# Performance work log

Measured on AMD Instinct MI355X. Metric: run time of the kernel, lower is better.

The kernel has to match this reference:

```python
import jax, jax.numpy as jnp
import numpy as np

H = 128        # hidden_dim
R = 50         # num_rbf
L = 4          # num_layers
CUTOFF = 5.0
N = 10000      # atoms
M = 64         # molecules
BOX = 54.7     # box side -> ~32 neighbors within cutoff
EPS = 1e-5     # LayerNorm eps (torch default)


def setup_inputs() -> dict:
    rng = np.random.default_rng(0)
    positions = rng.uniform(0.0, BOX, size=(N, 3)).astype(np.float32)
    # static radius graph (the torch module filters a dense NxN pair list by cutoff;
    # we do that once here so runtime shapes are fixed / jit-friendly)
    sq = (positions ** 2).sum(-1)
    d2 = sq[:, None] + sq[None, :] - 2.0 * positions @ positions.T
    mask = (d2 < CUTOFF * CUTOFF) & ~np.eye(N, dtype=bool)
    row, col = np.nonzero(mask)
    edge_index = jnp.asarray(np.stack([row, col]).astype(np.int32))  # [2, E]

    key = jax.random.key(0)
    ks = jax.random.split(key, 6)
    s = 0.05
    return dict(
        atomic_numbers=jax.random.randint(ks[0], (N,), 0, 100),
        positions=jnp.asarray(positions),
        batch=jnp.asarray((np.arange(N) * M // N).astype(np.int32)),  # sorted, all M present
        edge_index=edge_index,
        embedding=jax.random.normal(ks[1], (100, H), jnp.float32) * s,
        W1=jax.random.normal(ks[2], (L, H + R, H), jnp.float32) * s,
        b1=jnp.zeros((L, H), jnp.float32),
        W2=jax.random.normal(ks[3], (L, H, H), jnp.float32) * s,
        b2=jnp.zeros((L, H), jnp.float32),
        W_ih=jax.random.normal(ks[4], (L, H, 3 * H), jnp.float32) * s,
        b_ih=jax.random.normal(ks[5], (L, 3 * H), jnp.float32) * s,
        b_hh=jnp.zeros((L, 3 * H), jnp.float32),
        ln_g=jnp.ones((H,), jnp.float32),
        ln_b=jnp.zeros((H,), jnp.float32),
    )


def reference(atomic_numbers, positions, batch, edge_index, embedding,
              W1, b1, W2, b2, W_ih, b_ih, b_hh, ln_g, ln_b):
    x = embedding[jnp.clip(atomic_numbers, 0, 99)]                  # [N, H]
    row, col = edge_index[0], edge_index[1]
    d = jnp.linalg.norm(positions[row] - positions[col], axis=-1)   # [E]
    centers = jnp.linspace(0.0, CUTOFF, R)
    width = CUTOFF / R
    rbf = jnp.exp(-((d[:, None] - centers) ** 2) / (2.0 * width * width))  # [E, R]
    n_atoms = x.shape[0]
    for l in range(L):
        x_j = x[row]                                                # gather [E, H]
        inp = jnp.concatenate([x_j, rbf], axis=-1)                  # [E, H+R]
        msg = jax.nn.silu(inp @ W1[l] + b1[l]) @ W2[l] + b2[l]      # [E, H]
        aggr = jax.ops.segment_sum(msg, col, num_segments=n_atoms)  # [N, H]
        # GRU step with h0 = 0: W_hh @ h vanishes, only b_hh survives
        gi = aggr @ W_ih[l] + b_ih[l]                               # [N, 3H]
        gi_r, gi_z, gi_n = jnp.split(gi, 3, axis=-1)
        bh_r, bh_z, bh_n = jnp.split(b_hh[l], 3)
        r = jax.nn.sigmoid(gi_r + bh_r)
        z = jax.nn.sigmoid(gi_z + bh_z)
        n = jnp.tanh(gi_n + r * bh_n)
        x = x + (1.0 - z) * n                                       # h' = (1-z)*n + z*0
    mu = x.mean(-1, keepdims=True)
    var = ((x - mu) ** 2).mean(-1, keepdims=True)
    x = (x - mu) / jnp.sqrt(var + EPS) * ln_g + ln_b
    sums = jax.ops.segment_sum(x, batch, num_segments=M)            # [M, H]
    counts = jax.ops.segment_sum(jnp.ones((x.shape[0],), jnp.float32), batch, num_segments=M)
    graph_rep = sums / jnp.clip(counts, 1.0)[:, None]
    return x, graph_rep
```

## Files before the change

### kernel.cpp

```cpp
#include <hip/hip_runtime.h>
#include <hip/hip_bf16.h>
#include <math.h>


#define HH 128
#define RR 50
#define LL 4
#define L2E 1.4426950408889634f

typedef __attribute__((ext_vector_type(8))) short short8;
typedef __attribute__((ext_vector_type(4))) float floatx4;

__device__ __forceinline__ unsigned short f2bf(float f) {
    unsigned u = __float_as_uint(f);
    unsigned r = (u + 0x7fffu + ((u >> 16) & 1u)) >> 16;
    return (unsigned short)r;
}
__device__ __forceinline__ unsigned pack_bf2(float lo, float hi) {
    unsigned u0 = __float_as_uint(lo) + 0x8000u;
    unsigned u1 = __float_as_uint(hi) + 0x8000u;
    return __builtin_amdgcn_perm(u1, u0, 0x07060302);
}
__device__ __forceinline__ float fast_sigmoid(float x) {
    return __builtin_amdgcn_rcpf(1.f + __builtin_amdgcn_exp2f(x * (-L2E)));
}
__device__ __forceinline__ float fast_tanh(float x) {
    x = fminf(fmaxf(x, -15.f), 15.f);
    float t = __builtin_amdgcn_exp2f(x * (2.f * L2E));
    return (t - 1.f) * __builtin_amdgcn_rcpf(t + 1.f);
}
__device__ __forceinline__ int imin(int a, int b) { return a < b ? a : b; }

__global__ __launch_bounds__(256) void prep_kernel(
    const int* __restrict__ an, const float* __restrict__ emb,
    float* __restrict__ X,
    const float* __restrict__ pos, const int* __restrict__ erow,
    const int* __restrict__ ecol, float* __restrict__ dist,
    int* __restrict__ rowptr, int* __restrict__ bptr,
    const int* __restrict__ batch,
    const float* __restrict__ W1, unsigned short* __restrict__ W1rT,
    unsigned short* __restrict__ W1xT,
    const float* __restrict__ W2, const float* __restrict__ Wih,
    unsigned short* __restrict__ WcT,
    const float* __restrict__ b2, float* __restrict__ P,
    int N, int E, int M)
{
    int gidx = blockIdx.x * 256 + threadIdx.x;
    int c0 = N * HH;
    if (gidx < c0) {
        int i = gidx >> 7, n = gidx & 127;
        int z = an[i];
        z = z < 0 ? 0 : (z > 99 ? 99 : z);
        X[gidx] = emb[z * HH + n];
        return;
    }
    gidx -= c0;
    int PT = E > N ? E : N;
    if (gidx < PT) {
        int i = gidx;
        if (i < E) {
            int rc = erow[i];
            int rp = (i > 0) ? erow[i - 1] : -1;
            for (int r = rp + 1; r <= rc; ++r) rowptr[r] = i;
            if (i == E - 1)
                for (int r = rc + 1; r <= N; ++r) rowptr[r] = E;
        }
        if (i < N) {
            int bc = batch[i];
            int bp = (i > 0) ? batch[i - 1] : -1;
            for (int m = bp + 1; m <= bc; ++m) bptr[m] = i;
            if (i == N - 1)
                for (int m = bc + 1; m <= M; ++m) bptr[m] = N;
        }
        return;
    }
    gidx -= PT;
    if (gidx < E) {
        int e = gidx;
        int r = erow[e], c = ecol[e];
        float dx = pos[r * 3 + 0] - pos[c * 3 + 0];
        float dy = pos[r * 3 + 1] - pos[c * 3 + 1];
        float dz = pos[r * 3 + 2] - pos[c * 3 + 2];
        dist[e] = sqrtf(dx * dx + dy * dy + dz * dz);
        return;
    }
    gidx -= E;
    if (gidx < LL * HH * 64) {
        int l = gidx >> 13, rem = gidx & 8191;
        int f = rem >> 9, lane2 = (rem >> 3) & 63, j = rem & 7;
        int nt = f >> 1, h = f & 1;
        int n = nt * 16 + (lane2 & 15);
        int k = h * 32 + (lane2 >> 4) * 8 + j;
        float v = (k < RR) ? W1[((size_t)l * 178 + 128 + k) * HH + n] : 0.f;
        W1rT[gidx] = f2bf(v);
        return;
    }
    gidx -= LL * HH * 64;
    if (gidx < LL * HH * HH) {
        int l = gidx >> 14, rem = gidx & 16383, n = rem >> 7, k = rem & 127;
        W1xT[gidx] = f2bf(W1[((size_t)l * 178 + k) * HH + n]);
        return;
    }
    gidx -= LL * HH * HH;
    if (gidx < LL * HH * 384) {
        int l = gidx / (HH * 384), rem = gidx % (HH * 384);
        int i = rem / 384, j = rem % 384;
        const float* w2row = W2 + ((size_t)l * HH + i) * HH;
        const float* wih = Wih + (size_t)l * HH * 384;
        float acc = 0.f;
#pragma unroll 4
        for (int k = 0; k < HH; ++k)
            acc = fmaf(w2row[k], wih[(size_t)k * 384 + j], acc);
        WcT[((size_t)l * 384 + j) * HH + i] = f2bf(acc);
        return;
    }
    gidx -= LL * HH * 384;
    if (gidx < LL * 384) {
        int l = gidx / 384, j = gidx % 384;
        const float* b2l = b2 + (size_t)l * HH;
        const float* wih = Wih + (size_t)l * HH * 384;
        float acc = 0.f;
#pragma unroll 4
        for (int k = 0; k < HH; ++k)
            acc = fmaf(b2l[k], wih[(size_t)k * 384 + j], acc);
        P[gidx] = acc;
    }
}

#define XAB 32
__global__ __launch_bounds__(256) void xw_kernel(
    const float* __restrict__ X, const float* __restrict__ W,
    const float* __restrict__ bias, unsigned short* __restrict__ XWb, int N)
{
    __shared__ __align__(16) float A[XAB][HH];
    int tid = threadIdx.x;
    int abase = blockIdx.x * XAB;
    for (int idx = tid; idx < XAB * HH; idx += 256) {
        int a = idx >> 7, k = idx & 127;
        A[a][k] = (abase + a < N) ? X[(size_t)(abase + a) * HH + k] : 0.f;
    }
    __syncthreads();
    int n = tid & 127, s = tid >> 7;
    float acc[16];
#pragma unroll
    for (int i = 0; i < 16; ++i) acc[i] = 0.f;
    for (int kc = 0; kc < 32; ++kc) {
        float w0 = W[(4 * kc + 0) * HH + n];
        float w1 = W[(4 * kc + 1) * HH + n];
        float w2 = W[(4 * kc + 2) * HH + n];
        float w3 = W[(4 * kc + 3) * HH + n];
#pragma unroll
        for (int i = 0; i < 16; ++i) {
            float4 av = *(const float4*)&A[s * 16 + i][4 * kc];
            acc[i] = fmaf(av.x, w0, acc[i]);
            acc[i] = fmaf(av.y, w1, acc[i]);
            acc[i] = fmaf(av.z, w2, acc[i]);
            acc[i] = fmaf(av.w, w3, acc[i]);
        }
    }
    float b = bias[n];
#pragma unroll
    for (int i = 0; i < 16; ++i) {
        int a = abase + s * 16 + i;
        if (a < N) XWb[(size_t)a * HH + n] = f2bf(acc[i] + b);
    }
}

__global__ __launch_bounds__(256) void edge_mfma_kernel(
    const unsigned short* __restrict__ XWb, const unsigned short* __restrict__ W1rTf,
    const float* __restrict__ dist, const int* __restrict__ rowptr,
    const int* __restrict__ ecol, unsigned short* __restrict__ Sbf,
    int N, int nwaves)
{
    __shared__ __align__(16) unsigned short W1s[8192];
    int tid = threadIdx.x;
    {
        const uint4* src = (const uint4*)W1rTf;
        uint4* dst = (uint4*)W1s;
#pragma unroll
        for (int i = 0; i < 4; ++i) dst[tid + i * 256] = src[tid + i * 256];
    }
    __syncthreads();

    int wid = (blockIdx.x << 2) + (tid >> 6);
    int lane = tid & 63;
    int c = lane & 15, q = lane >> 4;

    const float stepc = 5.0f / 49.0f;
    const float negc = -50.f * L2E;
    float kqs = (float)(q << 3) * stepc;

    int NW = 2 * N;
    for (int w = wid; w < NW; w += nwaves) {
        int a = w >> 1, h = w & 1;
        int es = rowptr[a], ee = rowptr[a + 1];
        float acc[4][4];
#pragma unroll
        for (int t = 0; t < 4; ++t)
#pragma unroll
            for (int r = 0; r < 4; ++r) acc[t][r] = 0.f;

        if (es < ee) {
            int last = ee - 1;
            int ce0 = imin(es + c, last);
            float dcur = dist[ce0];
            int colcur = ecol[ce0];
            int ce1 = imin(es + 16 + c, last);
            float dnxt = dist[ce1];
            int colnxt = ecol[ce1];

            for (int eb = es; eb < ee; eb += 16) {
                const unsigned short* xwrow = XWb + (size_t)colcur * HH + h * 64;
                uint2 gx[4];
#pragma unroll
                for (int t = 0; t < 4; ++t)
                    gx[t] = *(const uint2*)&xwrow[t * 16 + (q << 2)];

                float d_t = dcur;
                dcur = dnxt; colcur = colnxt;
                int ce2 = imin(eb + 32 + c, last);
                dnxt = dist[ce2];
                colnxt = ecol[ce2];

                float dq0 = d_t - kqs;
                float dq1 = dq0 - 32.f * stepc;
                union { unsigned u[4]; short8 s; } ub0, ub1;
#pragma unroll
                for (int p = 0; p < 4; ++p) {
                    float t0 = dq0 - (float)(2 * p) * stepc;
                    float t1 = dq0 - (float)(2 * p + 1) * stepc;
                    float e0f = __builtin_amdgcn_exp2f(negc * t0 * t0);
                    float e1f = __builtin_amdgcn_exp2f(negc * t1 * t1);
                    ub0.u[p] = pack_bf2(e0f, e1f);
                    float t2 = dq1 - (float)(2 * p) * stepc;
                    float t3 = dq1 - (float)(2 * p + 1) * stepc;
                    float e2f = __builtin_amdgcn_exp2f(negc * t2 * t2);
                    float e3f = __builtin_amdgcn_exp2f(negc * t3 * t3);
                    ub1.u[p] = pack_bf2(e2f, e3f);
                }
                short8 B0 = ub0.s, B1 = ub1.s;
                float msk = ((eb + c) < ee) ? 1.f : 0.f;

                unsigned wbyte = (unsigned)(lane * 16);
                asm volatile("" : "+v"(wbyte));
                const char* Wlp = (const char*)W1s + wbyte;

#pragma unroll
                for (int t = 0; t < 4; ++t) {
                    int f0 = (h * 4 + t) * 2;
                    short8 A0 = *(const short8*)(Wlp + f0 * 1024);
                    short8 A1 = *(const short8*)(Wlp + (f0 + 1) * 1024);
                    floatx4 C;
                    C[0] = __uint_as_float(gx[t].x << 16);
                    C[1] = __uint_as_float(gx[t].x & 0xffff0000u);
                    C[2] = __uint_as_float(gx[t].y << 16);
                    C[3] = __uint_as_float(gx[t].y & 0xffff0000u);
                    C = __builtin_amdgcn_mfma_f32_16x16x32_bf16(A0, B0, C, 0, 0, 0);
                    C = __builtin_amdgcn_mfma_f32_16x16x32_bf16(A1, B1, C, 0, 0, 0);
#pragma unroll
                    for (int r = 0; r < 4; ++r) {
                        float hh = C[r];
                        float v = hh * fast_sigmoid(hh);
                        acc[t][r] = fmaf(v, msk, acc[t][r]);
                    }
                }
            }
        }

        int b0 = c & 1, b1 = (c >> 1) & 1, b2 = (c >> 2) & 1, b3 = (c >> 3) & 1;
        float s1[4][2];
#pragma unroll
        for (int t = 0; t < 4; ++t)
#pragma unroll
            for (int p = 0; p < 2; ++p) {
                float keep = b0 ? acc[t][2 * p + 1] : acc[t][2 * p];
                float send = b0 ? acc[t][2 * p] : acc[t][2 * p + 1];
                s1[t][p] = keep + __shfl_xor(send, 1, 64);
            }
        float s2[4];
#pragma unroll
        for (int t = 0; t < 4; ++t) {
            float keep = b1 ? s1[t][1] : s1[t][0];
            float send = b1 ? s1[t][0] : s1[t][1];
            s2[t] = keep + __shfl_xor(send, 2, 64);
        }
        float s3[2];
#pragma unroll
        for (int u = 0; u < 2; ++u) {
            float keep = b2 ? s2[2 * u + 1] : s2[2 * u];
            float send = b2 ? s2[2 * u] : s2[2 * u + 1];
            s3[u] = keep + __shfl_xor(send, 4, 64);
        }
        float keep = b3 ? s3[1] : s3[0];
        float send = b3 ? s3[0] : s3[1];
        float fin = keep + __shfl_xor(send, 8, 64);

        int t_fin = 2 * b3 + b2;
        int r_fin = 2 * b1 + b0;
        int n = t_fin * 16 + (q << 2) + r_fin;
        Sbf[(size_t)a * HH + h * 64 + n] = f2bf(fin);
    }
}

#define GA 16
__global__ __launch_bounds__(512) void grux_mfma_kernel(
    const unsigned short* __restrict__ Sbf, const unsigned short* __restrict__ WcT,
    const float* __restrict__ P, const float* __restrict__ bih,
    const float* __restrict__ bhh, const int* __restrict__ rowptr,
    float* __restrict__ X, int N,
    const unsigned short* __restrict__ W1xT, const float* __restrict__ b1next,
    unsigned short* __restrict__ XWb, int do_xw)
{
    __shared__ __align__(16) unsigned short Sb[GA][136];
    __shared__ __align__(16) unsigned short Xb[GA][136];
    int tid = threadIdx.x;
    int abase = blockIdx.x * GA;
    int w = tid >> 6, lane = tid & 63, c = lane & 15, q = lane >> 4;
    int n = w * 16 + c;

    float pn0 = P[n],        pn1 = P[128 + n],   pn2 = P[256 + n];
    float bi0 = bih[n],      bi1 = bih[128 + n], bi2 = bih[256 + n];
    float bh0 = bhh[n],      bh1 = bhh[128 + n], bh2 = bhh[256 + n];
    float deg[4];
#pragma unroll
    for (int r = 0; r < 4; ++r) {
        int a = abase + q * 4 + r;
        deg[r] = (a < N) ? (float)(rowptr[a + 1] - rowptr[a]) : 0.f;
    }

    if (tid < 128) {
        int a = tid >> 3, ch = tid & 7;
        int aa = abase + a; if (aa >= N) aa = N - 1;
        const uint4* src = (const uint4*)(Sbf + (size_t)aa * HH + ch * 16);
        uint4 v0 = src[0];
        uint4 v1 = src[1];
        uint4* dst = (uint4*)&Sb[a][ch * 16];
        dst[0] = v0;
        dst[1] = v1;
    }
    __syncthreads();

    floatx4 Cg0 = {0.f,0.f,0.f,0.f}, Cg1 = {0.f,0.f,0.f,0.f}, Cg2 = {0.f,0.f,0.f,0.f};
#pragma unroll
    for (int kt = 0; kt < 4; ++kt) {
        short8 A = *(const short8*)&Sb[c][kt * 32 + q * 8];
        short8 B0 = *(const short8*)&WcT[(size_t)(0 * 128 + n) * HH + kt * 32 + q * 8];
        short8 B1 = *(const short8*)&WcT[(size_t)(1 * 128 + n) * HH + kt * 32 + q * 8];
        short8 B2 = *(const short8*)&WcT[(size_t)(2 * 128 + n) * HH + kt * 32 + q * 8];
        Cg0 = __builtin_amdgcn_mfma_f32_16x16x32_bf16(A, B0, Cg0, 0, 0, 0);
        Cg1 = __builtin_amdgcn_mfma_f32_16x16x32_bf16(A, B1, Cg1, 0, 0, 0);
        Cg2 = __builtin_amdgcn_mfma_f32_16x16x32_bf16(A, B2, Cg2, 0, 0, 0);
    }

#pragma unroll
    for (int r = 0; r < 4; ++r) {
        int am = q * 4 + r;
        int a = abase + am;
        bool ok = a < N;
        float g0 = Cg0[r] + deg[r] * pn0 + bi0;
        float g1 = Cg1[r] + deg[r] * pn1 + bi1;
        float g2 = Cg2[r] + deg[r] * pn2 + bi2;
        float rr = fast_sigmoid(g0 + bh0);
        float zz = fast_sigmoid(g1 + bh1);
        float nn = fast_tanh(g2 + rr * bh2);
        float xv = 0.f;
        if (ok) {
            xv = X[(size_t)a * HH + n] + (1.f - zz) * nn;
            X[(size_t)a * HH + n] = xv;
        }
        Xb[am][n] = f2bf(xv);
    }

    if (!do_xw) return;
    __syncthreads();

    floatx4 Cx = {0.f, 0.f, 0.f, 0.f};
#pragma unroll
    for (int kt = 0; kt < 4; ++kt) {
        short8 A = *(const short8*)&Xb[c][kt * 32 + q * 8];
        short8 B = *(const short8*)&W1xT[(size_t)n * HH + kt * 32 + q * 8];
        Cx = __builtin_amdgcn_mfma_f32_16x16x32_bf16(A, B, Cx, 0, 0, 0);
    }
    float bn = b1next[n];
#pragma unroll
    for (int r = 0; r < 4; ++r) {
        int a = abase + q * 4 + r;
        if (a < N) XWb[(size_t)a * HH + n] = f2bf(Cx[r] + bn);
    }
}

__global__ __launch_bounds__(1024) void lnpool_kernel(
    const float* __restrict__ X, const float* __restrict__ g,
    const float* __restrict__ b, const int* __restrict__ bptr,
    float* __restrict__ outx, float* __restrict__ outg, int N)
{
    __shared__ float sm[16][128];
    int m = blockIdx.x, tid = threadIdx.x;
    int wv = tid >> 6, lane = tid & 63;
    int a0 = bptr[m], a1 = bptr[m + 1];
    float g0 = g[lane], g1 = g[64 + lane];
    float bb0 = b[lane], bb1 = b[64 + lane];
    float acc0 = 0.f, acc1 = 0.f;
    for (int a = a0 + wv; a < a1; a += 16) {
        float v0 = X[(size_t)a * HH + lane];
        float v1 = X[(size_t)a * HH + 64 + lane];
        float smv = v0 + v1;
        for (int off = 32; off > 0; off >>= 1) smv += __shfl_xor(smv, off, 64);
        float mu = smv * (1.f / 128.f);
        float d0 = v0 - mu, d1 = v1 - mu;
        float vq = d0 * d0 + d1 * d1;
        for (int off = 32; off > 0; off >>= 1) vq += __shfl_xor(vq, off, 64);
        float inv = rsqrtf(vq * (1.f / 128.f) + 1e-5f);
        float y0 = d0 * inv * g0 + bb0;
        float y1 = d1 * inv * g1 + bb1;
        outx[(size_t)a * HH + lane] = y0;
        outx[(size_t)a * HH + 64 + lane] = y1;
        acc0 += y0;
        acc1 += y1;
    }
    sm[wv][lane] = acc0;
    sm[wv][64 + lane] = acc1;
    __syncthreads();
    if (tid < 128) {
        float s = 0.f;
#pragma unroll
        for (int i = 0; i < 16; ++i) s += sm[i][tid];
        float cnt = (float)(a1 - a0);
        outg[(size_t)m * HH + tid] = s / fmaxf(cnt, 1.f);
    }
}

extern "C" void kernel_launch(void* const* d_in, const int* in_sizes, int n_in,
                              void* d_out, int out_size, void* d_ws, size_t ws_size,
                              hipStream_t stream)
{
    const int*   an   = (const int*)d_in[0];
    const float* pos  = (const float*)d_in[1];
    const int*   bat  = (const int*)d_in[2];
    const int*   eidx = (const int*)d_in[3];
    const float* emb  = (const float*)d_in[4];
    const float* W1   = (const float*)d_in[5];
    const float* b1   = (const float*)d_in[6];
    const float* W2   = (const float*)d_in[7];
    const float* b2   = (const float*)d_in[8];
    const float* Wih  = (const float*)d_in[9];
    const float* bih  = (const float*)d_in[10];
    const float* bhh  = (const float*)d_in[11];
    const float* lng  = (const float*)d_in[12];
    const float* lnb  = (const float*)d_in[13];

    int N = in_sizes[0];
    int E = in_sizes[3] / 2;
    int M = out_size / HH - N;
    const int* erow = eidx;
    const int* ecol = eidx + E;

    float* ws   = (float*)d_ws;
    size_t off = 0;
    float* X    = ws + off; off += (size_t)N * HH;
    unsigned short* Sbf = (unsigned short*)(ws + off); off += (size_t)N * HH / 2;
    unsigned short* XWb = (unsigned short*)(ws + off); off += (size_t)N * HH / 2;
    float* P    = ws + off; off += LL * 384;
    float* dist = ws + off; off += E;
    int* rowptr = (int*)(ws + off); off += N + 1;
    int* bptr   = (int*)(ws + off); off += M + 1;
    off = (off + 3) & ~(size_t)3;
    unsigned short* W1rT = (unsigned short*)(ws + off); off += (size_t)LL * HH * 32;
    unsigned short* W1xT = (unsigned short*)(ws + off); off += (size_t)LL * HH * 64;
    unsigned short* WcT  = (unsigned short*)(ws + off); off += (size_t)LL * 384 * 64;

    float* outx = (float*)d_out;
    float* outg = outx + (size_t)N * HH;

    int PT = (E > N ? E : N);
    long total = (long)N * HH + PT + E + LL * HH * 64 + LL * HH * HH
               + LL * HH * 384 + LL * 384;
    int prep_blocks = (int)((total + 255) / 256);

    prep_kernel<<<prep_blocks, 256, 0, stream>>>(
        an, emb, X, pos, erow, ecol, dist, rowptr, bptr, bat,
        W1, W1rT, W1xT, W2, Wih, WcT, b2, P, N, E, M);

    xw_kernel<<<(N + XAB - 1) / XAB, 256, 0, stream>>>(X, W1, b1, XWb, N);

    int eblocks = (2 * N + 3) / 4;
    int nwaves = eblocks * 4;
    int grux_blocks = (N + GA - 1) / GA;
    for (int l = 0; l < LL; ++l) {
        edge_mfma_kernel<<<eblocks, 256, 0, stream>>>(
            XWb, W1rT + (size_t)l * HH * 64, dist, rowptr, ecol, Sbf, N, nwaves);
        int do_xw = (l < LL - 1) ? 1 : 0;
        int ln = (l + 1 < LL) ? l + 1 : l;
        grux_mfma_kernel<<<grux_blocks, 512, 0, stream>>>(
            Sbf, WcT + (size_t)l * 384 * HH, P + l * 384,
            bih + l * 384, bhh + l * 384, rowptr, X, N,
            W1xT + (size_t)ln * HH * HH, b1 + (size_t)ln * HH, XWb, do_xw);
    }

    lnpool_kernel<<<M, 1024, 0, stream>>>(X, lng, lnb, bptr, outx, outg, N);
}
```

Baseline: 319.5 us.

## Fuse edge message kernel with GRU update into one per-layer kernel

Merges the edge aggregation kernel and the GRU/next-layer projection kernel into a single kernel per layer. Each 512-thread block handles 4 atoms, keeping the aggregated messages in shared memory instead of writing them to global memory, and ping-pongs the XW buffers across layers. This removes one launch per layer and the global round-trip of the aggregate. In exchange, the MFMA GRU stage now does 16-row tiles where only 4 rows are valid, and the W1 tile is reloaded into shared memory by four times as many blocks.

```diff
diff --git a/kernel.cpp b/kernel.cpp
--- a/kernel.cpp
+++ b/kernel.cpp
@@ -166,179 +166,163 @@
     }
 }
 
-__global__ __launch_bounds__(256) void edge_mfma_kernel(
-    const unsigned short* __restrict__ XWb, const unsigned short* __restrict__ W1rTf,
+__global__ __launch_bounds__(512) void fused_layer_kernel(
+    const unsigned short* __restrict__ XWin, const unsigned short* __restrict__ W1rTf,
     const float* __restrict__ dist, const int* __restrict__ rowptr,
-    const int* __restrict__ ecol, unsigned short* __restrict__ Sbf,
-    int N, int nwaves)
+    const int* __restrict__ ecol,
+    const unsigned short* __restrict__ WcT, const float* __restrict__ P,
+    const float* __restrict__ bih, const float* __restrict__ bhh,
+    float* __restrict__ X,
+    const unsigned short* __restrict__ W1xT, const float* __restrict__ b1next,
+    unsigned short* __restrict__ XWout, int do_xw, int N)
 {
     __shared__ __align__(16) unsigned short W1s[8192];
+    __shared__ __align__(16) unsigned short Sb[16][136];
+    __shared__ __align__(16) unsigned short Xb[16][136];
     int tid = threadIdx.x;
+    int abase = blockIdx.x * 4;
+    int w = tid >> 6, lane = tid & 63;
+    int c = lane & 15, q = lane >> 4;
+
     {
         const uint4* src = (const uint4*)W1rTf;
         uint4* dst = (uint4*)W1s;
-#pragma unroll
-        for (int i = 0; i < 4; ++i) dst[tid + i * 256] = src[tid + i * 256];
+        dst[tid] = src[tid];
+        dst[tid + 512] = src[tid + 512];
+        if (tid < 204) {
+            uint4 z; z.x = 0; z.y = 0; z.z = 0; z.w = 0;
+            ((uint4*)&Sb[4][0])[tid] = z;
+        }
     }
     __syncthreads();
 
-    int wid = (blockIdx.x << 2) + (tid >> 6);
-    int lane = tid & 63;
-    int c = lane & 15, q = lane >> 4;
-
-    const float stepc = 5.0f / 49.0f;
-    const float negc = -50.f * L2E;
-    float kqs = (float)(q << 3) * stepc;
-
-    int NW = 2 * N;
-    for (int w = wid; w < NW; w += nwaves) {
-        int a = w >> 1, h = w & 1;
-        int es = rowptr[a], ee = rowptr[a + 1];
+    {
+        int al = w >> 1, h = w & 1;
+        int a = abase + al;
         float acc[4][4];
 #pragma unroll
         for (int t = 0; t < 4; ++t)
 #pragma unroll
             for (int r = 0; r < 4; ++r) acc[t][r] = 0.f;
 
-        if (es < ee) {
-            int last = ee - 1;
-            int ce0 = imin(es + c, last);
-            float dcur = dist[ce0];
-            int colcur = ecol[ce0];
-            int ce1 = imin(es + 16 + c, last);
-            float dnxt = dist[ce1];
-            int colnxt = ecol[ce1];
-
-            for (int eb = es; eb < ee; eb += 16) {
-                const unsigned short* xwrow = XWb + (size_t)colcur * HH + h * 64;
-                uint2 gx[4];
-#pragma unroll
-                for (int t = 0; t < 4; ++t)
-                    gx[t] = *(const uint2*)&xwrow[t * 16 + (q << 2)];
-
-                float d_t = dcur;
-                dcur = dnxt; colcur = colnxt;
-                int ce2 = imin(eb + 32 + c, last);
-                dnxt = dist[ce2];
-                colnxt = ecol[ce2];
-
-                float dq0 = d_t - kqs;
-                float dq1 = dq0 - 32.f * stepc;
-                union { unsigned u[4]; short8 s; } ub0, ub1;
-#pragma unroll
-                for (int p = 0; p < 4; ++p) {
-                    float t0 = dq0 - (float)(2 * p) * stepc;
-                    float t1 = dq0 - (float)(2 * p + 1) * stepc;
-                    float e0f = __builtin_amdgcn_exp2f(negc * t0 * t0);
-                    float e1f = __builtin_amdgcn_exp2f(negc * t1 * t1);
-                    ub0.u[p] = pack_bf2(e0f, e1f);
-                    float t2 = dq1 - (float)(2 * p) * stepc;
-                    float t3 = dq1 - (float)(2 * p + 1) * stepc;
-                    float e2f = __builtin_amdgcn_exp2f(negc * t2 * t2);
-                    float e3f = __builtin_amdgcn_exp2f(negc * t3 * t3);
-                    ub1.u[p] = pack_bf2(e2f, e3f);
-                }
-                short8 B0 = ub0.s, B1 = ub1.s;
-                float msk = ((eb + c) < ee) ? 1.f : 0.f;
-
-                unsigned wbyte = (unsigned)(lane * 16);
-                asm volatile("" : "+v"(wbyte));
-                const char* Wlp = (const char*)W1s + wbyte;
-
-#pragma unroll
-                for (int t = 0; t < 4; ++t) {
-                    int f0 = (h * 4 + t) * 2;
-                    short8 A0 = *(const short8*)(Wlp + f0 * 1024);
-                    short8 A1 = *(const short8*)(Wlp + (f0 + 1) * 1024);
-                    floatx4 C;
-                    C[0] = __uint_as_float(gx[t].x << 16);
-                    C[1] = __uint_as_float(gx[t].x & 0xffff0000u);
-                    C[2] = __uint_as_float(gx[t].y << 16);
-                    C[3] = __uint_as_float(gx[t].y & 0xffff0000u);
-                    C = __builtin_amdgcn_mfma_f32_16x16x32_bf16(A0, B0, C, 0, 0, 0);
-                    C = __builtin_amdgcn_mfma_f32_16x16x32_bf16(A1, B1, C, 0, 0, 0);
-#pragma unroll
-                    for (int r = 0; r < 4; ++r) {
-                        float hh = C[r];
-                        float v = hh * fast_sigmoid(hh);
-                        acc[t][r] = fmaf(v, msk, acc[t][r]);
+        if (a < N) {
+            int es = rowptr[a], ee = rowptr[a + 1];
+            const float stepc = 5.0f / 49.0f;
+            const float negc = -50.f * L2E;
+            float kqs = (float)(q << 3) * stepc;
+            if (es < ee) {
+                int last = ee - 1;
+                int ce0 = imin(es + c, last);
+                float dcur = dist[ce0];
+                int colcur = ecol[ce0];
+                int ce1 = imin(es + 16 + c, last);
+                float dnxt = dist[ce1];
+                int colnxt = ecol[ce1];
+
+                for (int eb = es; eb < ee; eb += 16) {
+                    const unsigned short* xwrow = XWin + (size_t)colcur * HH + h * 64;
+                    uint2 gx[4];
+#pragma unroll
+                    for (int t = 0; t < 4; ++t)
+                        gx[t] = *(const uint2*)&xwrow[t * 16 + (q << 2)];
+
+                    float d_t = dcur;
+                    dcur = dnxt; colcur = colnxt;
+                    int ce2 = imin(eb + 32 + c, last);
+                    dnxt = dist[ce2];
+                    colnxt = ecol[ce2];
+
+                    float dq0 = d_t - kqs;
+                    float dq1 = dq0 - 32.f * stepc;
+                    union { unsigned u[4]; short8 s; } ub0, ub1;
+#pragma unroll
+                    for (int p = 0; p < 4; ++p) {
+                        float t0 = dq0 - (float)(2 * p) * stepc;
+                        float t1 = dq0 - (float)(2 * p + 1) * stepc;
+                        float e0f = __builtin_amdgcn_exp2f(negc * t0 * t0);
+                        float e1f = __builtin_amdgcn_exp2f(negc * t1 * t1);
+                        ub0.u[p] = pack_bf2(e0f, e1f);
+                        float t2 = dq1 - (float)(2 * p) * stepc;
+                        float t3 = dq1 - (float)(2 * p + 1) * stepc;
+                        float e2f = __builtin_amdgcn_exp2f(negc * t2 * t2);
+                        float e3f = __builtin_amdgcn_exp2f(negc * t3 * t3);
+                        ub1.u[p] = pack_bf2(e2f, e3f);
+                    }
+                    short8 B0 = ub0.s, B1 = ub1.s;
+                    float msk = ((eb + c) < ee) ? 1.f : 0.f;
+
+                    unsigned wbyte = (unsigned)(lane * 16);
+                    asm volatile("" : "+v"(wbyte));
+                    const char* Wlp = (const char*)W1s + wbyte;
+
+#pragma unroll
+                    for (int t = 0; t < 4; ++t) {
+                        int f0 = (h * 4 + t) * 2;
+                        short8 A0 = *(const short8*)(Wlp + f0 * 1024);
+                        short8 A1 = *(const short8*)(Wlp + (f0 + 1) * 1024);
+                        floatx4 C;
+                        C[0] = __uint_as_float(gx[t].x << 16);
+                        C[1] = __uint_as_float(gx[t].x & 0xffff0000u);
+                        C[2] = __uint_as_float(gx[t].y << 16);
+                        C[3] = __uint_as_float(gx[t].y & 0xffff0000u);
+                        C = __builtin_amdgcn_mfma_f32_16x16x32_bf16(A0, B0, C, 0, 0, 0);
+                        C = __builtin_amdgcn_mfma_f32_16x16x32_bf16(A1, B1, C, 0, 0, 0);
+#pragma unroll
+                        for (int r = 0; r < 4; ++r) {
+                            float hh = C[r];
+                            float v = hh * fast_sigmoid(hh);
+                            acc[t][r] = fmaf(v, msk, acc[t][r]);
+                        }
                     }
                 }
             }
-        }
-
-        int b0 = c & 1, b1 = (c >> 1) & 1, b2 = (c >> 2) & 1, b3 = (c >> 3) & 1;
-        float s1[4][2];
-#pragma unroll
-        for (int t = 0; t < 4; ++t)
-#pragma unroll
-            for (int p = 0; p < 2; ++p) {
-                float keep = b0 ? acc[t][2 * p + 1] : acc[t][2 * p];
-                float send = b0 ? acc[t][2 * p] : acc[t][2 * p + 1];
-                s1[t][p] = keep + __shfl_xor(send, 1, 64);
+            int b0 = c & 1, b1 = (c >> 1) & 1, b2 = (c >> 2) & 1, b3 = (c >> 3) & 1;
+            float s1[4][2];
+#pragma unroll
+            for (int t = 0; t < 4; ++t)
+#pragma unroll
+                for (int p = 0; p < 2; ++p) {
+                    float keep = b0 ? acc[t][2 * p + 1] : acc[t][2 * p];
+                    float send = b0 ? acc[t][2 * p] : acc[t][2 * p + 1];
+                    s1[t][p] = keep + __shfl_xor(send, 1, 64);
+                }
+            float s2[4];
+#pragma unroll
+            for (int t = 0; t < 4; ++t) {
+                float keep = b1 ? s1[t][1] : s1[t][0];
+                float send = b1 ? s1[t][0] : s1[t][1];
+                s2[t] = keep + __shfl_xor(send, 2, 64);
             }
-        float s2[4];
-#pragma unroll
-        for (int t = 0; t < 4; ++t) {
-            float keep = b1 ? s1[t][1] : s1[t][0];
-            float send = b1 ? s1[t][0] : s1[t][1];
-            s2[t] = keep + __shfl_xor(send, 2, 64);
-        }
-        float s3[2];
-#pragma unroll
-        for (int u = 0; u < 2; ++u) {
-            float keep = b2 ? s2[2 * u + 1] : s2[2 * u];
-            float send = b2 ? s2[2 * u] : s2[2 * u + 1];
-            s3[u] = keep + __shfl_xor(send, 4, 64);
-        }
-        float keep = b3 ? s3[1] : s3[0];
-        float send = b3 ? s3[0] : s3[1];
-        float fin = keep + __shfl_xor(send, 8, 64);
-
-        int t_fin = 2 * b3 + b2;
-        int r_fin = 2 * b1 + b0;
-        int n = t_fin * 16 + (q << 2) + r_fin;
-        Sbf[(size_t)a * HH + h * 64 + n] = f2bf(fin);
-    }
-}
-
-#define GA 16
-__global__ __launch_bounds__(512) void grux_mfma_kernel(
-    const unsigned short* __restrict__ Sbf, const unsigned short* __restrict__ WcT,
-    const float* __restrict__ P, const float* __restrict__ bih,
-    const float* __restrict__ bhh, const int* __restrict__ rowptr,
-    float* __restrict__ X, int N,
-    const unsigned short* __restrict__ W1xT, const float* __restrict__ b1next,
-    unsigned short* __restrict__ XWb, int do_xw)
-{
-    __shared__ __align__(16) unsigned short Sb[GA][136];
-    __shared__ __align__(16) unsigned short Xb[GA][136];
-    int tid = threadIdx.x;
-    int abase = blockIdx.x * GA;
-    int w = tid >> 6, lane = tid & 63, c = lane & 15, q = lane >> 4;
+            float s3[2];
+#pragma unroll
+            for (int u = 0; u < 2; ++u) {
+                float keep = b2 ? s2[2 * u + 1] : s2[2 * u];
+                float send = b2 ? s2[2 * u] : s2[2 * u + 1];
+                s3[u] = keep + __shfl_xor(send, 4, 64);
+            }
+            float keep = b3 ? s3[1] : s3[0];
+            float send = b3 ? s3[0] : s3[1];
+            float fin = keep + __shfl_xor(send, 8, 64);
+
+            int t_fin = 2 * b3 + b2;
+            int r_fin = 2 * b1 + b0;
+            int n = t_fin * 16 + (q << 2) + r_fin;
+            Sb[al][h * 64 + n] = f2bf(fin);
+        }
+    }
+    __syncthreads();
+
     int n = w * 16 + c;
-
-    float pn0 = P[n],        pn1 = P[128 + n],   pn2 = P[256 + n];
-    float bi0 = bih[n],      bi1 = bih[128 + n], bi2 = bih[256 + n];
-    float bh0 = bhh[n],      bh1 = bhh[128 + n], bh2 = bhh[256 + n];
+    float pn0 = P[n],   pn1 = P[128 + n],   pn2 = P[256 + n];
+    float bi0 = bih[n], bi1 = bih[128 + n], bi2 = bih[256 + n];
+    float bh0 = bhh[n], bh1 = bhh[128 + n], bh2 = bhh[256 + n];
     float deg[4];
 #pragma unroll
     for (int r = 0; r < 4; ++r) {
-        int a = abase + q * 4 + r;
-        deg[r] = (a < N) ? (float)(rowptr[a + 1] - rowptr[a]) : 0.f;
-    }
-
-    if (tid < 128) {
-        int a = tid >> 3, ch = tid & 7;
-        int aa = abase + a; if (aa >= N) aa = N - 1;
-        const uint4* src = (const uint4*)(Sbf + (size_t)aa * HH + ch * 16);
-        uint4 v0 = src[0];
-        uint4 v1 = src[1];
-        uint4* dst = (uint4*)&Sb[a][ch * 16];
-        dst[0] = v0;
-        dst[1] = v1;
-    }
-    __syncthreads();
+        int am = q * 4 + r;
+        int a = abase + am;
+        deg[r] = (am < 4 && a < N) ? (float)(rowptr[a + 1] - rowptr[a]) : 0.f;
+    }
 
     floatx4 Cg0 = {0.f,0.f,0.f,0.f}, Cg1 = {0.f,0.f,0.f,0.f}, Cg2 = {0.f,0.f,0.f,0.f};
 #pragma unroll
@@ -356,7 +340,7 @@
     for (int r = 0; r < 4; ++r) {
         int am = q * 4 + r;
         int a = abase + am;
-        bool ok = a < N;
+        bool ok = (am < 4) && (a < N);
         float g0 = Cg0[r] + deg[r] * pn0 + bi0;
         float g1 = Cg1[r] + deg[r] * pn1 + bi1;
         float g2 = Cg2[r] + deg[r] * pn2 + bi2;
@@ -384,8 +368,9 @@
     float bn = b1next[n];
 #pragma unroll
     for (int r = 0; r < 4; ++r) {
-        int a = abase + q * 4 + r;
-        if (a < N) XWb[(size_t)a * HH + n] = f2bf(Cx[r] + bn);
+        int am = q * 4 + r;
+        int a = abase + am;
+        if (am < 4 && a < N) XWout[(size_t)a * HH + n] = f2bf(Cx[r] + bn);
     }
 }
 
@@ -458,8 +443,8 @@
     float* ws   = (float*)d_ws;
     size_t off = 0;
     float* X    = ws + off; off += (size_t)N * HH;
-    unsigned short* Sbf = (unsigned short*)(ws + off); off += (size_t)N * HH / 2;
-    unsigned short* XWb = (unsigned short*)(ws + off); off += (size_t)N * HH / 2;
+    unsigned short* XW0 = (unsigned short*)(ws + off); off += (size_t)N * HH / 2;
+    unsigned short* XW1 = (unsigned short*)(ws + off); off += (size_t)N * HH / 2;
     float* P    = ws + off; off += LL * 384;
     float* dist = ws + off; off += E;
     int* rowptr = (int*)(ws + off); off += N + 1;
@@ -481,20 +466,21 @@
         an, emb, X, pos, erow, ecol, dist, rowptr, bptr, bat,
         W1, W1rT, W1xT, W2, Wih, WcT, b2, P, N, E, M);
 
-    xw_kernel<<<(N + XAB - 1) / XAB, 256, 0, stream>>>(X, W1, b1, XWb, N);
-
-    int eblocks = (2 * N + 3) / 4;
-    int nwaves = eblocks * 4;
-    int grux_blocks = (N + GA - 1) / GA;
+    xw_kernel<<<(N + XAB - 1) / XAB, 256, 0, stream>>>(X, W1, b1, XW0, N);
+
+    int fblocks = (N + 3) / 4;
+    unsigned short* xin = XW0;
+    unsigned short* xout = XW1;
     for (int l = 0; l < LL; ++l) {
-        edge_mfma_kernel<<<eblocks, 256, 0, stream>>>(
-            XWb, W1rT + (size_t)l * HH * 64, dist, rowptr, ecol, Sbf, N, nwaves);
         int do_xw = (l < LL - 1) ? 1 : 0;
         int ln = (l + 1 < LL) ? l + 1 : l;
-        grux_mfma_kernel<<<grux_blocks, 512, 0, stream>>>(
-            Sbf, WcT + (size_t)l * 384 * HH, P + l * 384,
-            bih + l * 384, bhh + l * 384, rowptr, X, N,
-            W1xT + (size_t)ln * HH * HH, b1 + (size_t)ln * HH, XWb, do_xw);
+        fused_layer_kernel<<<fblocks, 512, 0, stream>>>(
+            xin, W1rT + (size_t)l * HH * 64, dist, rowptr, ecol,
+            WcT + (size_t)l * 384 * HH, P + l * 384,
+            bih + l * 384, bhh + l * 384, X,
+            W1xT + (size_t)ln * HH * HH, b1 + (size_t)ln * HH,
+            xout, do_xw, N);
+        unsigned short* tmp = xin; xin = xout; xout = tmp;
     }
 
     lnpool_kernel<<<M, 1024, 0, stream>>>(X, lng, lnb, bptr, outx, outg, N);
```

After: 434.9 us. 36.1% more time.
